# Kernel tuning notes

Hardware: AMD Instinct MI355X
Metric: run time of the kernel (lower is better)

The kernel has to match this reference:

```python
import jax, jax.numpy as jnp
import numpy as np

PRE_NMS_TOPK = 6000
POST_NMS_TOPK = 1000
NMS_THRESH = 0.7
MIN_SIZE = 16.0
NEG = -1e9  # stand-in for -inf that is safe under autodiff


def setup_inputs() -> dict:
    key = jax.random.key(0)
    k1, k2, k3, k4, k5, k6, k7, k8 = jax.random.split(key, 8)
    B, A = 8, 200000
    N = B * A
    # realistic anchors: centers within a ~1333x800 canvas, sizes 16..256
    cx = jax.random.uniform(k1, (N,), minval=0.0, maxval=1200.0)
    cy = jax.random.uniform(k2, (N,), minval=0.0, maxval=800.0)
    w = jax.random.uniform(k3, (N,), minval=16.0, maxval=256.0)
    h = jax.random.uniform(k4, (N,), minval=16.0, maxval=256.0)
    anchors = jnp.stack([cx - 0.5 * w, cy - 0.5 * h, cx + 0.5 * w, cy + 0.5 * h], axis=1)
    batch_indices = jnp.sort(jax.random.randint(k5, (N,), 0, B)).astype(jnp.int32)
    image_sizes = jax.random.randint(k6, (B, 2), 600, 1334).astype(jnp.int32)  # (H, W)
    objectness_logits = jax.random.normal(k7, (N, 1), dtype=jnp.float32)
    bbox_deltas = jax.random.normal(k8, (N, 4), dtype=jnp.float32) * 0.2
    return {
        'anchors': anchors,
        'batch_indices': batch_indices,
        'image_sizes': image_sizes,
        'objectness_logits': objectness_logits,
        'bbox_deltas': bbox_deltas,
    }


def _nms_one(bx, sc):
    """Greedy NMS on [K,4] boxes / [K] scores; returns POST_NMS_TOPK (idx, ok)."""
    K = bx.shape[0]
    areas = (bx[:, 2] - bx[:, 0]) * (bx[:, 3] - bx[:, 1])
    ar = jnp.arange(K)

    def step(sup, _):
        s = jnp.where(sup, NEG, sc)
        j = jnp.argmax(s)
        ok = s[j] > 0.5 * NEG
        b = bx[j]
        ix1 = jnp.maximum(b[0], bx[:, 0])
        iy1 = jnp.maximum(b[1], bx[:, 1])
        ix2 = jnp.minimum(b[2], bx[:, 2])
        iy2 = jnp.minimum(b[3], bx[:, 3])
        inter = jnp.maximum(ix2 - ix1, 0.0) * jnp.maximum(iy2 - iy1, 0.0)
        iou = inter / (areas + areas[j] - inter + 1e-9)
        sup = sup | (iou > NMS_THRESH) | (ar == j)
        return sup, (j, ok)

    sup0 = sc <= 0.5 * NEG  # padded / invalid entries start suppressed
    _, (idx, ok) = jax.lax.scan(step, sup0, None, length=POST_NMS_TOPK)
    return idx, ok


def reference(anchors, batch_indices, image_sizes, objectness_logits, bbox_deltas):
    B = image_sizes.shape[0]
    N = anchors.shape[0]
    sizes = image_sizes[batch_indices].astype(jnp.float32)  # [N,2] (H,W) per anchor

    # --- box decode ---
    a_w = anchors[:, 2] - anchors[:, 0]
    a_h = anchors[:, 3] - anchors[:, 1]
    a_x = anchors[:, 0] + 0.5 * a_w
    a_y = anchors[:, 1] + 0.5 * a_h
    t_x, t_y = bbox_deltas[:, 0], bbox_deltas[:, 1]
    t_w, t_h = bbox_deltas[:, 2], bbox_deltas[:, 3]
    p_x = a_x + t_x * a_w
    p_y = a_y + t_y * a_h
    p_w = a_w * jnp.exp(jnp.clip(t_w, -10.0, 10.0))
    p_h = a_h * jnp.exp(jnp.clip(t_h, -10.0, 10.0))
    x1 = p_x - 0.5 * p_w
    y1 = p_y - 0.5 * p_h
    x2 = p_x + 0.5 * p_w
    y2 = p_y + 0.5 * p_h

    # --- clip to image ---
    H, W = sizes[:, 0], sizes[:, 1]
    x1 = jnp.clip(x1, 0.0, W - 1.0)
    y1 = jnp.clip(y1, 0.0, H - 1.0)
    x2 = jnp.clip(x2, 0.0, W - 1.0)
    y2 = jnp.clip(y2, 0.0, H - 1.0)
    boxes = jnp.stack([x1, y1, x2, y2], axis=1)  # [N,4]

    # --- min-size filter (as score masking) ---
    valid = ((x2 - x1) >= MIN_SIZE) & ((y2 - y1) >= MIN_SIZE)
    fg = jax.nn.sigmoid(objectness_logits[:, 0])

    # --- per-image top-k over masked scores ---
    img_mask = batch_indices[None, :] == jnp.arange(B, dtype=batch_indices.dtype)[:, None]  # [B,N]
    scores = jnp.where(img_mask & valid[None, :], fg[None, :], NEG)  # [B,N]
    top_scores, top_idx = jax.lax.top_k(scores, PRE_NMS_TOPK)  # [B,PRE]
    top_boxes = boxes[top_idx]  # [B,PRE,4]

    # --- NMS per image ---
    keep_idx, keep_ok = jax.vmap(_nms_one)(top_boxes, top_scores)  # [B,POST]

    sel = jnp.take_along_axis(top_idx, keep_idx, axis=1)  # global anchor indices [B,POST]
    okf = keep_ok[..., None].astype(boxes.dtype)
    props = jnp.take_along_axis(top_boxes, keep_idx[..., None], axis=1) * okf  # [B,POST,4]
    obj = objectness_logits[sel] * okf  # [B,POST,1]
    deltas_out = bbox_deltas[sel] * okf  # [B,POST,4]
    bidx = jnp.where(keep_ok, jnp.arange(B, dtype=jnp.int32)[:, None], -1)  # [B,POST]

    return (props.reshape(-1, 4), bidx.reshape(-1), obj.reshape(-1, 1),
            deltas_out.reshape(-1, 4), keep_ok.reshape(-1))
```

## Files before the change

### kernel.cpp

```cpp
#include <hip/hip_runtime.h>
#include <stdint.h>

#define PRE_K   6000
#define POST_K  1000
#define CAP     8192
#define BINS    1024
#define ROWS    6016
#define CH      94
#define JSPLIT  8
#define NEGF    -1000000000.0f
#define IOU_EPS 16.0f


__device__ __forceinline__ uint32_t orderf(float f) {
  uint32_t u = __float_as_uint(f);
  return (u & 0x80000000u) ? ~u : (u | 0x80000000u);
}

__device__ __forceinline__ int score_bin(float sc) {
  int bin = (int)floorf((sc + 12.0f) * ((float)BINS / 24.0f));
  return bin < 0 ? 0 : (bin > BINS - 1 ? BINS - 1 : bin);
}

__device__ __forceinline__ int bin_slot(int bin) {
  return ((bin & 15) << 6) | (bin >> 4);
}

__device__ __forceinline__ void decode_box(
    const float* __restrict__ anchors, const float* __restrict__ deltas,
    const int* __restrict__ isz, int n, int b,
    double& x1, double& y1, double& x2, double& y2, bool& valid) {
  double ax1 = (double)anchors[4 * n + 0], ay1 = (double)anchors[4 * n + 1];
  double ax2 = (double)anchors[4 * n + 2], ay2 = (double)anchors[4 * n + 3];
  double aw = ax2 - ax1, ah = ay2 - ay1;
  double acx = ax1 + 0.5 * aw, acy = ay1 + 0.5 * ah;
  double tx = (double)deltas[4 * n + 0], ty = (double)deltas[4 * n + 1];
  double tw = (double)deltas[4 * n + 2], th = (double)deltas[4 * n + 3];
  tw = tw < -10.0 ? -10.0 : (tw > 10.0 ? 10.0 : tw);
  th = th < -10.0 ? -10.0 : (th > 10.0 ? 10.0 : th);
  double px = acx + tx * aw, py = acy + ty * ah;
  double pw = aw * exp(tw), ph = ah * exp(th);
  double H = (double)isz[2 * b + 0], W = (double)isz[2 * b + 1];
  double wm = W - 1.0, hm = H - 1.0;
  x1 = px - 0.5 * pw; y1 = py - 0.5 * ph;
  x2 = px + 0.5 * pw; y2 = py + 0.5 * ph;
  x1 = fmin(fmax(x1, 0.0), wm); x2 = fmin(fmax(x2, 0.0), wm);
  y1 = fmin(fmax(y1, 0.0), hm); y2 = fmin(fmax(y2, 0.0), hm);
  valid = (x2 - x1 >= 16.0) && (y2 - y1 >= 16.0);
}

__device__ __forceinline__ bool iou_exact(const double* __restrict__ tbox,
                                          const double* __restrict__ tarea,
                                          size_t ri, size_t ci) {
  const double* pr = &tbox[ri * 4];
  const double* pc = &tbox[ci * 4];
  double w = fmin(pr[2], pc[2]) - fmax(pr[0], pc[0]); w = w > 0.0 ? w : 0.0;
  double h = fmin(pr[3], pc[3]) - fmax(pr[1], pc[1]); h = h > 0.0 ? h : 0.0;
  double it = w * h;
  return it > 0.7 * (tarea[ri] + tarea[ci] - it + 1e-9);
}


__global__ void __launch_bounds__(256) k_score(const float* __restrict__ anchors,
                                               const int* __restrict__ bix,
                                               const int* __restrict__ isz,
                                               const float* __restrict__ logits,
                                               const float* __restrict__ deltas,
                                               float* __restrict__ scores,
                                               uint32_t* __restrict__ hist, int N) {
  const int SPAN = 4096;
  int start = blockIdx.x * SPAN;
  int end = start + SPAN < N ? start + SPAN : N;
  __shared__ uint32_t lh[2][BINS];
  for (int i = threadIdx.x; i < 2 * BINS; i += 256) ((uint32_t*)lh)[i] = 0u;
  __shared__ int s_b0, s_b1;
  if (threadIdx.x == 0) { s_b0 = bix[start]; s_b1 = bix[end - 1]; }
  __syncthreads();
  int b0 = s_b0, b1 = s_b1;

  for (int n = start + (int)threadIdx.x; n < end; n += 256) {
    int b = bix[n];
    double x1, y1, x2, y2; bool valid;
    decode_box(anchors, deltas, isz, n, b, x1, y1, x2, y2, valid);
    float sc = valid ? logits[n] : NEGF;
    scores[n] = sc;
    if (valid) {
      int bin = score_bin(sc);
      if (b == b0)      atomicAdd(&lh[0][bin], 1u);
      else if (b == b1) atomicAdd(&lh[1][bin], 1u);
      else              atomicAdd(&hist[b * BINS + bin_slot(bin)], 1u);
    }
  }
  __syncthreads();
  for (int bin = threadIdx.x; bin < BINS; bin += 256) {
    uint32_t c0 = lh[0][bin];
    if (c0) atomicAdd(&hist[b0 * BINS + bin_slot(bin)], c0);
    if (b1 != b0) {
      uint32_t c1 = lh[1][bin];
      if (c1) atomicAdd(&hist[b1 * BINS + bin_slot(bin)], c1);
    }
  }
}

__global__ void __launch_bounds__(1024) k_compact(const float* __restrict__ scores,
                                                  const int* __restrict__ bix,
                                                  const uint32_t* __restrict__ hist,
                                                  uint32_t* __restrict__ cnt,
                                                  uint64_t* __restrict__ cand, int N) {
  const int SPAN = 8192;
  int start = blockIdx.x * SPAN;
  int end = start + SPAN < N ? start + SPAN : N;
  int t = threadIdx.x;
  __shared__ int s_b0, s_b1;
  __shared__ uint32_t sh[BINS];
  __shared__ int s_bs;
  __shared__ uint32_t lcnt[8], lbase[8];
  if (t == 0) { s_b0 = bix[start]; s_b1 = bix[end - 1]; }
  if (t < 8) lcnt[t] = 0u;
  __syncthreads();
  int b0 = s_b0, b1 = s_b1;

  uint32_t bs0 = 0, bs1 = 0;
  for (int pass = 0; pass < 2; pass++) {
    int b = pass == 0 ? b0 : b1;
    if (pass == 1 && b1 == b0) { bs1 = bs0; break; }
    if (t < BINS) sh[t] = hist[b * BINS + bin_slot(t)];
    if (t == 0) s_bs = 0;
    __syncthreads();
    for (int off = 1; off < BINS; off <<= 1) {
      uint32_t v = (t < BINS && t + off < BINS) ? sh[t + off] : 0u;
      __syncthreads();
      if (t < BINS) sh[t] += v;
      __syncthreads();
    }
    if (t < BINS && sh[t] >= PRE_K) atomicMax(&s_bs, t);
    __syncthreads();
    if (pass == 0) bs0 = (uint32_t)s_bs; else bs1 = (uint32_t)s_bs;
    __syncthreads();
  }

  bool     predv[8];
  uint64_t keyv[8];
  uint32_t lposv[8];
  int      bv[8];
  int nt = 0;
  for (int base = start; base < end; base += 1024, nt++) {
    int n = base + t;
    bool pred = false; int b = 0; uint64_t key = 0ull; uint32_t lp = 0u;
    if (n < end) {
      float sc = scores[n];
      if (sc > 0.5f * NEGF) {
        b = bix[n];
        uint32_t bs = (b == b0) ? bs0 : bs1;
        if ((uint32_t)score_bin(sc) >= bs) {
          pred = true;
          key = ((uint64_t)orderf(sc) << 32) | (uint64_t)(uint32_t)(~(uint32_t)n);
          lp = atomicAdd(&lcnt[b], 1u);
        }
      }
    }
    predv[nt] = pred; keyv[nt] = key; lposv[nt] = lp; bv[nt] = b;
  }
  __syncthreads();
  if (t < 8) {
    uint32_t c = lcnt[t];
    lbase[t] = c ? atomicAdd(&cnt[t], c) : 0u;
  }
  __syncthreads();
  for (int k = 0; k < nt; k++) {
    if (predv[k]) {
      uint32_t pos = lbase[bv[k]] + lposv[k];
      if (pos < CAP) cand[(size_t)bv[k] * CAP + pos] = keyv[k];
    }
  }
}

__global__ void __launch_bounds__(256) k_rank(const uint64_t* __restrict__ cand,
                                              const uint32_t* __restrict__ cnt,
                                              uint32_t* __restrict__ prank) {
  int blk = blockIdx.x;
  int js = blk % JSPLIT;
  int ic = (blk / JSPLIT) % 32;
  int b  = blk / (JSPLIT * 32);
  int t = threadIdx.x;
  int C = (int)min(cnt[b], (uint32_t)CAP);
  if (ic * 256 >= C) return;
  const uint64_t* g = cand + (size_t)b * CAP;
  int i = ic * 256 + t;
  uint64_t ki = (i < C) ? g[i] : 0ull;

  int q = (C + JSPLIT - 1) / JSPLIT;
  int j0 = js * q;
  int j1 = j0 + q < C ? j0 + q : C;

  __shared__ uint64_t tile[1024];
  int rank = 0;
  for (int base = j0; base < j1; base += 1024) {
#pragma unroll
    for (int u = 0; u < 4; u++) {
      int j = base + u * 256 + t;
      tile[u * 256 + t] = (j < j1) ? g[j] : 0ull;
    }
    __syncthreads();
    int lim = j1 - base < 1024 ? j1 - base : 1024;
    const ulonglong2* t2 = (const ulonglong2*)tile;
    int pairs = lim >> 1;
    int jj = 0;
    for (; jj + 4 <= pairs; jj += 4) {
      ulonglong2 v0 = t2[jj + 0], v1 = t2[jj + 1];
      ulonglong2 v2 = t2[jj + 2], v3 = t2[jj + 3];
      rank += (v0.x > ki) ? 1 : 0; rank += (v0.y > ki) ? 1 : 0;
      rank += (v1.x > ki) ? 1 : 0; rank += (v1.y > ki) ? 1 : 0;
      rank += (v2.x > ki) ? 1 : 0; rank += (v2.y > ki) ? 1 : 0;
      rank += (v3.x > ki) ? 1 : 0; rank += (v3.y > ki) ? 1 : 0;
    }
    for (; jj < pairs; jj++) {
      ulonglong2 v = t2[jj];
      rank += (v.x > ki) ? 1 : 0; rank += (v.y > ki) ? 1 : 0;
    }
    if (lim & 1) rank += (tile[lim - 1] > ki) ? 1 : 0;
    __syncthreads();
  }
  if (i < C) prank[((size_t)b * JSPLIT + js) * CAP + i] = (uint32_t)rank;
}

__global__ void __launch_bounds__(256) k_place_gather(
    const uint64_t* __restrict__ cand, const uint32_t* __restrict__ cnt,
    const uint32_t* __restrict__ prank,
    const float* __restrict__ anchors, const float* __restrict__ deltas,
    const int* __restrict__ isz,
    double* __restrict__ tbox, double* __restrict__ tarea,
    float4* __restrict__ tboxf, float* __restrict__ tareaf,
    int* __restrict__ top_n, int* __restrict__ Cnum, int B) {
  int idx = blockIdx.x * blockDim.x + threadIdx.x;
  if (idx >= B * CAP) return;
  int b = idx / CAP, i = idx % CAP;
  int C = (int)min(cnt[b], (uint32_t)CAP);
  if (i == 0) Cnum[b] = C < PRE_K ? C : PRE_K;
  if (i >= C) return;
  uint32_t rank = 0;
#pragma unroll
  for (int js = 0; js < JSPLIT; js++)
    rank += prank[((size_t)b * JSPLIT + js) * CAP + i];
  if (rank >= PRE_K) return;
  int n = (int)(~(uint32_t)(cand[idx] & 0xFFFFFFFFull));
  double x1, y1, x2, y2; bool valid;
  decode_box(anchors, deltas, isz, n, b, x1, y1, x2, y2, valid);
  size_t row = (size_t)b * ROWS + rank;
  tbox[row * 4 + 0] = x1;
  tbox[row * 4 + 1] = y1;
  tbox[row * 4 + 2] = x2;
  tbox[row * 4 + 3] = y2;
  double ar = (x2 - x1) * (y2 - y1);
  tarea[row] = ar;
  tboxf[row] = make_float4((float)x1, (float)y1, (float)x2, (float)y2);
  tareaf[row] = (float)ar;
  top_n[b * PRE_K + rank] = n;
}

__global__ void __launch_bounds__(64) k_iou_mat(const float4* __restrict__ tboxf,
                                                const float* __restrict__ tareaf,
                                                const double* __restrict__ tbox,
                                                const double* __restrict__ tarea,
                                                const int* __restrict__ Cnum,
                                                uint32_t* __restrict__ maskT) {
  int rc = blockIdx.x;
  int cc = blockIdx.y;
  int b  = blockIdx.z;
  if (rc > cc) return;
  int C = Cnum[b];
  if (cc * 64 >= C) return;
  int lane = threadIdx.x;
  size_t bb = (size_t)b * ROWS;

  float4 cb4 = tboxf[bb + (size_t)cc * 64 + lane];
  float  sca = 0.7f * tareaf[bb + (size_t)cc * 64 + lane];
  __shared__ float4 rbx[64];
  __shared__ float  rsa[64];
  rbx[lane] = tboxf[bb + (size_t)rc * 64 + lane];
  rsa[lane] = 0.7f * tareaf[bb + (size_t)rc * 64 + lane];
  __syncthreads();

  bool isdiag = (rc == cc);
  uint32_t res0 = 0u, res1 = 0u;

  for (int i = 0; i < 64; i++) {
    float4 r4 = rbx[i];
    float sra = rsa[i];
    float iw = fminf(r4.z, cb4.z) - fmaxf(r4.x, cb4.x);
    float ih = fminf(r4.w, cb4.w) - fmaxf(r4.y, cb4.y);
    iw = fmaxf(iw, 0.0f); ih = fmaxf(ih, 0.0f);
    float inter = iw * ih;
    float diff = fmaf(1.7f, inter, -(sra + sca));
    bool gt = isdiag ? (lane > i) : true;
    unsigned long long sup   = __ballot(gt && (diff >  IOU_EPS));
    unsigned long long loose = __ballot(gt && (diff > -IOU_EPS));
    unsigned long long border = loose & ~sup;
    if (border) {
      bool mine = (border >> lane) & 1ull;
      bool ex = false;
      if (mine)
        ex = iou_exact(tbox, tarea, bb + (size_t)rc * 64 + i,
                       bb + (size_t)cc * 64 + lane);
      sup |= __ballot(ex);
    }
    if (lane == i) { res0 = (uint32_t)sup; res1 = (uint32_t)(sup >> 32); }
  }
  uint2* seg = (uint2*)(maskT + (((size_t)b * CH + cc) * ROWS + (size_t)rc * 64) * 2);
  seg[lane] = make_uint2(res0, res1);
}

__global__ void __launch_bounds__(256) k_nms_reduce(const uint32_t* __restrict__ maskT,
                                                    const double* __restrict__ tbox,
                                                    const int* __restrict__ Cnum,
                                                    const int* __restrict__ top_n,
                                                    const float* __restrict__ logits,
                                                    const float* __restrict__ deltas,
                                                    float* __restrict__ out, int B) {
  int b = blockIdx.x, t = threadIdx.x;
  int wave = t >> 6, lane = t & 63;
  int C = Cnum[b];
  int nch = (C + 63) >> 6;
  const uint32_t* Mb = maskT + (size_t)b * CH * ROWS * 2;
  size_t bb = (size_t)b * ROWS;

  __shared__ uint32_t acc[CH][2];
  __shared__ uint16_t kept[POST_K];
  __shared__ uint16_t pend[2][64];
  __shared__ int      npend[2];
  __shared__ uint64_t s_kept;

  for (int i = t; i < CH * 2; i += 256) ((uint32_t*)acc)[i] = 0u;
  if (t < 2) npend[t] = 0;
  __syncthreads();

  uint2 dgv = make_uint2(0u, 0u), pfv = make_uint2(0u, 0u);
  if (wave == 0 && nch > 0) {
    const uint2* pd = (const uint2*)(Mb + ((size_t)0 * ROWS + lane) * 2);
    dgv = pd[0];
    if (nch > 1) {
      const uint2* pp = (const uint2*)(Mb + ((size_t)1 * ROWS + lane) * 2);
      pfv = pp[0];
    }
  }

  int nkept = 0;
  for (int c = 0; c < nch; c++) {
    int par = c & 1;
    int base = c << 6;

    if (wave == 0) {
      uint64_t sup = (uint64_t)acc[c][0] | ((uint64_t)acc[c][1] << 32);
      int rem = C - base;
      if (rem < 64) sup |= ~((1ull << rem) - 1ull);
      uint64_t diag = (uint64_t)dgv.x | ((uint64_t)dgv.y << 32);
      uint64_t keptMask = 0ull;
      uint64_t alive = ~sup;
      uint64_t m = alive;
      while (m) {
        int i = __builtin_ctzll(m);
        keptMask |= 1ull << i;
        uint64_t d = (uint64_t)__shfl((long long)diag, i, 64);
        sup |= d | (1ull << i);
        m = alive & ~sup;
      }
      int allowed = POST_K - nkept;
      int pc2 = __popcll(keptMask);
      while (pc2 > allowed) {
        keptMask &= ~(1ull << (63 - __builtin_clzll(keptMask)));
        pc2--;
      }
      if (lane == 0) { s_kept = keptMask; npend[par ^ 1] = pc2; }
      if ((keptMask >> lane) & 1ull) {
        int pfx = __popcll(keptMask & ((1ull << lane) - 1ull));
        kept[nkept + pfx] = (uint16_t)(base + lane);
        pend[par ^ 1][pfx] = (uint16_t)(base + lane);
      }
      if (c + 1 < nch) {
        uint32_t v0 = ((keptMask >> lane) & 1ull) ? pfv.x : 0u;
        uint32_t v1 = ((keptMask >> lane) & 1ull) ? pfv.y : 0u;
#pragma unroll
        for (int off = 32; off > 0; off >>= 1) {
          v0 |= (uint32_t)__shfl_xor((int)v0, off, 64);
          v1 |= (uint32_t)__shfl_xor((int)v1, off, 64);
        }
        if (lane == 0) {
          if (v0) atomicOr(&acc[c + 1][0], v0);
          if (v1) atomicOr(&acc[c + 1][1], v1);
        }
        const uint2* pd = (const uint2*)(Mb + (((size_t)(c + 1)) * ROWS + base + 64 + lane) * 2);
        dgv = pd[0];
        if (c + 2 < nch) {
          const uint2* pp = (const uint2*)(Mb + (((size_t)(c + 2)) * ROWS + base + 64 + lane) * 2);
          pfv = pp[0];
        }
      }
    } else {
      int np = npend[par];
      int cc0 = c + 1;
      int span = nch - cc0;
      if (np > 0 && span > 0) {
        int total = np * span;
        for (int it = t - 64; it < total; it += 192) {
          int pi = it / span;
          int cc = cc0 + (it - pi * span);
          int row = (int)pend[par][pi];
          const uint2* pm = (const uint2*)(Mb + ((size_t)cc * ROWS + row) * 2);
          uint2 mv = pm[0];
          if (mv.x) atomicOr(&acc[cc][0], mv.x);
          if (mv.y) atomicOr(&acc[cc][1], mv.y);
        }
      }
    }
    __syncthreads();

    int pc = __popcll(s_kept);
    nkept += pc;
    if (nkept >= POST_K) break;
  }

  __syncthreads();
  int M_out = B * POST_K;
  for (int s2 = t; s2 < POST_K; s2 += 256) {
    float p0 = 0.f, p1 = 0.f, p2 = 0.f, p3 = 0.f;
    float ob = 0.f, d0f = 0.f, d1f = 0.f, d2f = 0.f, d3f = 0.f;
    float bi = -1.0f, okv = 0.0f;
    if (s2 < nkept) {
      int j = (int)kept[s2];
      int n = top_n[b * PRE_K + j];
      const double* p = &tbox[(bb + j) * 4];
      p0 = (float)p[0]; p1 = (float)p[1]; p2 = (float)p[2]; p3 = (float)p[3];
      ob = logits[n];
      d0f = deltas[4 * n + 0]; d1f = deltas[4 * n + 1];
      d2f = deltas[4 * n + 2]; d3f = deltas[4 * n + 3];
      bi = (float)b; okv = 1.0f;
    }
    int idx = b * POST_K + s2;
    out[idx * 4 + 0] = p0;
    out[idx * 4 + 1] = p1;
    out[idx * 4 + 2] = p2;
    out[idx * 4 + 3] = p3;
    out[4 * M_out + idx] = bi;
    out[5 * M_out + idx] = ob;
    out[6 * M_out + idx * 4 + 0] = d0f;
    out[6 * M_out + idx * 4 + 1] = d1f;
    out[6 * M_out + idx * 4 + 2] = d2f;
    out[6 * M_out + idx * 4 + 3] = d3f;
    out[10 * M_out + idx] = okv;
  }
}


extern "C" void kernel_launch(void* const* d_in, const int* in_sizes, int n_in,
                              void* d_out, int out_size, void* d_ws, size_t ws_size,
                              hipStream_t stream) {
  const float* anchors = (const float*)d_in[0];
  const int*   bix     = (const int*)d_in[1];
  const int*   isz     = (const int*)d_in[2];
  const float* logits  = (const float*)d_in[3];
  const float* deltas  = (const float*)d_in[4];
  float* out = (float*)d_out;

  int N = in_sizes[1];
  int B = in_sizes[2] / 2;

  uintptr_t p = (uintptr_t)d_ws;
  double*   tbox   = (double*)p;    p += (size_t)B * ROWS * 4 * sizeof(double);
  double*   tarea  = (double*)p;    p += (size_t)B * ROWS * sizeof(double);
  uint64_t* cand   = (uint64_t*)p;  p += (size_t)B * CAP * sizeof(uint64_t);
  float*    scores = (float*)p;     p += (size_t)N * sizeof(float);
  uint32_t* hist   = (uint32_t*)p;  p += (size_t)B * BINS * sizeof(uint32_t);
  uint32_t* cnt    = (uint32_t*)p;  p += (size_t)B * sizeof(uint32_t);
  uint32_t* prank  = (uint32_t*)p;  p += (size_t)B * JSPLIT * CAP * sizeof(uint32_t);
  int*      top_n    = (int*)p;     p += (size_t)B * PRE_K * sizeof(int);
  int*      Cnum     = (int*)p;      p += (size_t)B * sizeof(int);
  p = (p + 255) & ~(uintptr_t)255;
  uint32_t* maskT    = (uint32_t*)p; p += (size_t)B * CH * ROWS * 2 * sizeof(uint32_t);
  float4*   tboxf  = (float4*)scores;
  float*    tareaf = (float*)(scores + (size_t)B * ROWS * 4);
  (void)ws_size; (void)n_in; (void)out_size;

  hipMemsetAsync(hist, 0, (size_t)(B * BINS + B) * sizeof(uint32_t), stream);
  k_score<<<(N + 4095) / 4096, 256, 0, stream>>>(anchors, bix, isz, logits, deltas,
                                                 scores, hist, N);
  k_compact<<<(N + 8191) / 8192, 1024, 0, stream>>>(scores, bix, hist, cnt, cand, N);
  k_rank<<<B * 32 * JSPLIT, 256, 0, stream>>>(cand, cnt, prank);
  k_place_gather<<<(B * CAP + 255) / 256, 256, 0, stream>>>(cand, cnt, prank,
                                                            anchors, deltas, isz,
                                                            tbox, tarea, tboxf,
                                                            tareaf, top_n, Cnum, B);
  dim3 iou_grid(CH, CH, B);
  k_iou_mat<<<iou_grid, 64, 0, stream>>>(tboxf, tareaf, tbox, tarea, Cnum, maskT);
  k_nms_reduce<<<B, 256, 0, stream>>>(maskT, tbox, Cnum, top_n, logits, deltas,
                                      out, B);
}
```

Measured before the change: 419.2 us.

## Deepen NMS reduce pipeline with register-staged mask loads and per-lane IoU rows

The IoU-matrix kernel now gives each lane one row box and loops over column boxes from shared memory. Each lane builds its own 64-bit suppression word, which replaces two ballots per step and the cooperative border check. The NMS reduce kernel has wave 0 look two chunks ahead, with a second prefetch register and OR-ing into acc[c+2]. The helper waves load the pending kept rows' mask words into KREG registers one iteration ahead and apply the atomics in the next iteration, so global-load latency is hidden behind the serial chunk scan. The costs are more registers and more complex pipeline bookkeeping, and the exact IoU path is now taken divergently per lane.

```diff
diff --git a/kernel.cpp b/kernel.cpp
--- a/kernel.cpp
+++ b/kernel.cpp
@@ -10,6 +10,7 @@
 #define JSPLIT  8
 #define NEGF    -1000000000.0f
 #define IOU_EPS 16.0f
+#define KREG    12
 
 
 __device__ __forceinline__ uint32_t orderf(float f) {
@@ -273,38 +274,32 @@
   int lane = threadIdx.x;
   size_t bb = (size_t)b * ROWS;
 
-  float4 cb4 = tboxf[bb + (size_t)cc * 64 + lane];
-  float  sca = 0.7f * tareaf[bb + (size_t)cc * 64 + lane];
-  __shared__ float4 rbx[64];
-  __shared__ float  rsa[64];
-  rbx[lane] = tboxf[bb + (size_t)rc * 64 + lane];
-  rsa[lane] = 0.7f * tareaf[bb + (size_t)rc * 64 + lane];
+  float4 rb4 = tboxf[bb + (size_t)rc * 64 + lane];
+  float  sra = 0.7f * tareaf[bb + (size_t)rc * 64 + lane];
+  __shared__ float4 cbx[64];
+  __shared__ float  csa[64];
+  cbx[lane] = tboxf[bb + (size_t)cc * 64 + lane];
+  csa[lane] = 0.7f * tareaf[bb + (size_t)cc * 64 + lane];
   __syncthreads();
 
   bool isdiag = (rc == cc);
   uint32_t res0 = 0u, res1 = 0u;
 
-  for (int i = 0; i < 64; i++) {
-    float4 r4 = rbx[i];
-    float sra = rsa[i];
-    float iw = fminf(r4.z, cb4.z) - fmaxf(r4.x, cb4.x);
-    float ih = fminf(r4.w, cb4.w) - fmaxf(r4.y, cb4.y);
+  for (int j = 0; j < 64; j++) {
+    float4 c4 = cbx[j];
+    float sca = csa[j];
+    float iw = fminf(c4.z, rb4.z) - fmaxf(c4.x, rb4.x);
+    float ih = fminf(c4.w, rb4.w) - fmaxf(c4.y, rb4.y);
     iw = fmaxf(iw, 0.0f); ih = fmaxf(ih, 0.0f);
     float inter = iw * ih;
     float diff = fmaf(1.7f, inter, -(sra + sca));
-    bool gt = isdiag ? (lane > i) : true;
-    unsigned long long sup   = __ballot(gt && (diff >  IOU_EPS));
-    unsigned long long loose = __ballot(gt && (diff > -IOU_EPS));
-    unsigned long long border = loose & ~sup;
-    if (border) {
-      bool mine = (border >> lane) & 1ull;
-      bool ex = false;
-      if (mine)
-        ex = iou_exact(tbox, tarea, bb + (size_t)rc * 64 + i,
-                       bb + (size_t)cc * 64 + lane);
-      sup |= __ballot(ex);
-    }
-    if (lane == i) { res0 = (uint32_t)sup; res1 = (uint32_t)(sup >> 32); }
+    bool gt = isdiag ? (j > lane) : true;
+    bool sup = gt && (diff > IOU_EPS);
+    if (gt && !sup && diff > -IOU_EPS) {
+      sup = iou_exact(tbox, tarea, bb + (size_t)rc * 64 + lane,
+                      bb + (size_t)cc * 64 + j);
+    }
+    if (sup) { if (j < 32) res0 |= 1u << j; else res1 |= 1u << (j & 31); }
   }
   uint2* seg = (uint2*)(maskT + (((size_t)b * CH + cc) * ROWS + (size_t)rc * 64) * 2);
   seg[lane] = make_uint2(res0, res1);
@@ -334,22 +329,22 @@
   if (t < 2) npend[t] = 0;
   __syncthreads();
 
-  uint2 dgv = make_uint2(0u, 0u), pfv = make_uint2(0u, 0u);
+  uint2 dgv = make_uint2(0u, 0u), pfv = make_uint2(0u, 0u), pfv2 = make_uint2(0u, 0u);
   if (wave == 0 && nch > 0) {
-    const uint2* pd = (const uint2*)(Mb + ((size_t)0 * ROWS + lane) * 2);
-    dgv = pd[0];
-    if (nch > 1) {
-      const uint2* pp = (const uint2*)(Mb + ((size_t)1 * ROWS + lane) * 2);
-      pfv = pp[0];
-    }
-  }
+    dgv = *(const uint2*)(Mb + ((size_t)0 * ROWS + lane) * 2);
+    if (nch > 1) pfv  = *(const uint2*)(Mb + ((size_t)1 * ROWS + lane) * 2);
+    if (nch > 2) pfv2 = *(const uint2*)(Mb + ((size_t)2 * ROWS + lane) * 2);
+  }
+
+  uint2 lz[KREG];
+#pragma unroll
+  for (int u = 0; u < KREG; u++) lz[u] = make_uint2(0u, 0u);
+  int lz_total = 0, lz_cc0 = 0, lz_span = 1;
 
   int nkept = 0;
   for (int c = 0; c < nch; c++) {
-    int par = c & 1;
-    int base = c << 6;
-
     if (wave == 0) {
+      int base = c << 6;
       uint64_t sup = (uint64_t)acc[c][0] | ((uint64_t)acc[c][1] << 32);
       int rem = C - base;
       if (rem < 64) sup |= ~((1ull << rem) - 1ull);
@@ -370,46 +365,80 @@
         keptMask &= ~(1ull << (63 - __builtin_clzll(keptMask)));
         pc2--;
       }
-      if (lane == 0) { s_kept = keptMask; npend[par ^ 1] = pc2; }
-      if ((keptMask >> lane) & 1ull) {
+      if (lane == 0) { s_kept = keptMask; npend[c & 1] = pc2; }
+      bool mine = (keptMask >> lane) & 1ull;
+      if (mine) {
         int pfx = __popcll(keptMask & ((1ull << lane) - 1ull));
         kept[nkept + pfx] = (uint16_t)(base + lane);
-        pend[par ^ 1][pfx] = (uint16_t)(base + lane);
+        pend[c & 1][pfx] = (uint16_t)(base + lane);
       }
       if (c + 1 < nch) {
-        uint32_t v0 = ((keptMask >> lane) & 1ull) ? pfv.x : 0u;
-        uint32_t v1 = ((keptMask >> lane) & 1ull) ? pfv.y : 0u;
+        uint32_t v0 = mine ? pfv.x : 0u, v1 = mine ? pfv.y : 0u;
+        uint32_t w0 = mine ? pfv2.x : 0u, w1 = mine ? pfv2.y : 0u;
 #pragma unroll
         for (int off = 32; off > 0; off >>= 1) {
           v0 |= (uint32_t)__shfl_xor((int)v0, off, 64);
           v1 |= (uint32_t)__shfl_xor((int)v1, off, 64);
+          w0 |= (uint32_t)__shfl_xor((int)w0, off, 64);
+          w1 |= (uint32_t)__shfl_xor((int)w1, off, 64);
         }
         if (lane == 0) {
           if (v0) atomicOr(&acc[c + 1][0], v0);
           if (v1) atomicOr(&acc[c + 1][1], v1);
+          if (c + 2 < nch) {
+            if (w0) atomicOr(&acc[c + 2][0], w0);
+            if (w1) atomicOr(&acc[c + 2][1], w1);
+          }
         }
-        const uint2* pd = (const uint2*)(Mb + (((size_t)(c + 1)) * ROWS + base + 64 + lane) * 2);
-        dgv = pd[0];
-        if (c + 2 < nch) {
-          const uint2* pp = (const uint2*)(Mb + (((size_t)(c + 2)) * ROWS + base + 64 + lane) * 2);
-          pfv = pp[0];
+        int nb = base + 64;
+        dgv = *(const uint2*)(Mb + (((size_t)(c + 1)) * ROWS + nb + lane) * 2);
+        if (c + 2 < nch) pfv  = *(const uint2*)(Mb + (((size_t)(c + 2)) * ROWS + nb + lane) * 2);
+        else             pfv  = make_uint2(0u, 0u);
+        if (c + 3 < nch) pfv2 = *(const uint2*)(Mb + (((size_t)(c + 3)) * ROWS + nb + lane) * 2);
+        else             pfv2 = make_uint2(0u, 0u);
+      }
+    } else {
+      if (lz_total > 0) {
+#pragma unroll
+        for (int u = 0; u < KREG; u++) {
+          int it = (t - 64) + u * 192;
+          if (it < lz_total) {
+            int pi = it / lz_span;
+            int cc = lz_cc0 + (it - pi * lz_span);
+            if (lz[u].x) atomicOr(&acc[cc][0], lz[u].x);
+            if (lz[u].y) atomicOr(&acc[cc][1], lz[u].y);
+          }
         }
       }
-    } else {
-      int np = npend[par];
-      int cc0 = c + 1;
+      int np = (c >= 1) ? npend[(c - 1) & 1] : 0;
+      int cc0 = c + 2;
       int span = nch - cc0;
       if (np > 0 && span > 0) {
         int total = np * span;
-        for (int it = t - 64; it < total; it += 192) {
+#pragma unroll
+        for (int u = 0; u < KREG; u++) {
+          int it = (t - 64) + u * 192;
+          uint2 v = make_uint2(0u, 0u);
+          if (it < total) {
+            int pi = it / span;
+            int cc = cc0 + (it - pi * span);
+            int row = (int)pend[(c - 1) & 1][pi];
+            v = *(const uint2*)(Mb + ((size_t)cc * ROWS + row) * 2);
+          }
+          lz[u] = v;
+        }
+        for (int it = (t - 64) + KREG * 192; it < total; it += 192) {
           int pi = it / span;
           int cc = cc0 + (it - pi * span);
-          int row = (int)pend[par][pi];
-          const uint2* pm = (const uint2*)(Mb + ((size_t)cc * ROWS + row) * 2);
-          uint2 mv = pm[0];
-          if (mv.x) atomicOr(&acc[cc][0], mv.x);
-          if (mv.y) atomicOr(&acc[cc][1], mv.y);
+          int row = (int)pend[(c - 1) & 1][pi];
+          uint2 v = *(const uint2*)(Mb + ((size_t)cc * ROWS + row) * 2);
+          if (v.x) atomicOr(&acc[cc][0], v.x);
+          if (v.y) atomicOr(&acc[cc][1], v.y);
         }
+        lz_total = total < KREG * 192 ? total : KREG * 192;
+        lz_cc0 = cc0; lz_span = span;
+      } else {
+        lz_total = 0;
       }
     }
     __syncthreads();
```

Measured after the change: 385.4 us. 8.1% less time.
